# Optimization experiments

Measured on AMD Instinct MI355X. Metric: run time of the kernel, lower is better.

Reference implementation:

```python
import jax, jax.numpy as jnp
import numpy as np

N_NODES = 100000
N_EDGES = 640000
IN_FEATS = 128
OUT_FEATS = 128


def setup_inputs() -> dict:
    key = jax.random.key(0)
    k1, k2, k3 = jax.random.split(key, 3)
    feat = jax.random.normal(k1, (N_NODES, IN_FEATS), dtype=jnp.float32)
    edge_src = jax.random.randint(k2, (N_EDGES,), 0, N_NODES, dtype=jnp.int64)
    edge_dst = jax.random.randint(k3, (N_EDGES,), 0, N_NODES, dtype=jnp.int64)
    # init.constant_(weight, 1) / init.constant_(bias, 1) in the original module
    weight = jnp.ones((OUT_FEATS, IN_FEATS), dtype=jnp.float32)
    bias = jnp.ones((OUT_FEATS,), dtype=jnp.float32)
    return {"feat": feat, "edge_src": edge_src, "edge_dst": edge_dst,
            "weight": weight, "bias": bias}


def reference(feat, edge_src, edge_dst, weight, bias):
    # copy_u: message on each edge is the source node's feature  [E, F_in]
    msgs = feat[edge_src]
    # sum reduce messages into destination nodes                 [N_V, F_in]
    h = jax.ops.segment_sum(msgs, edge_dst, num_segments=N_NODES)
    # linear: h @ W^T + b                                        [N_V, F_out]
    return h @ weight.T + bias
```

## Files before the change

kernel.cpp:

```cpp
#include <hip/hip_runtime.h>

#define F 128
#define STRIDE 64

typedef __bf16 bf8 __attribute__((ext_vector_type(8)));
typedef __bf16 bf4 __attribute__((ext_vector_type(4)));
typedef float f4 __attribute__((ext_vector_type(4)));
typedef unsigned short us8 __attribute__((ext_vector_type(8)));

__global__ void zero_int(int* __restrict__ p, int n) {
  int i = blockIdx.x * blockDim.x + threadIdx.x;
  if (i < n) p[i] = 0;
}

__global__ void zero_f4(float4* __restrict__ p, int n4) {
  int i = blockIdx.x * blockDim.x + threadIdx.x;
  if (i < n4) p[i] = make_float4(0.f, 0.f, 0.f, 0.f);
}

__global__ __launch_bounds__(256, 2) void transform_and_build(
    const float* __restrict__ feat, const float* __restrict__ W,
    __bf16* __restrict__ tf, const int* __restrict__ esrc,
    const int* __restrict__ edst, int* __restrict__ cnt,
    int* __restrict__ bucket, int n_rows, int n_groups, int t_blocks,
    int b_blocks, int nE) {
  __shared__ bf8 wlds[2048];
  const int tid = threadIdx.x;

  if ((int)blockIdx.x >= t_blocks) {
    const int bbid = blockIdx.x - t_blocks;
    for (int e = bbid * 256 + tid; e < nE; e += b_blocks * 256) {
      int d = edst[e];
      int pos = atomicAdd(&cnt[d], 1);
      if (pos < STRIDE) bucket[(size_t)d * STRIDE + pos] = esrc[e];
    }
    return;
  }

  const int lane = tid & 63;
  const int wid = tid >> 6;
  const int lr = lane & 15;
  const int hi = lane >> 4;
  const int lk = hi * 8;

#pragma unroll
  for (int i = 0; i < 8; ++i) {
    int fid = tid + i * 256;
    int fl = fid & 63;
    int kkt = fid >> 6;
    int kk = kkt & 3;
    int t = kkt >> 2;
    const float* wr = W + (size_t)(t * 16 + (fl & 15)) * F + kk * 32 + (fl >> 4) * 8;
    float4 u0 = *(const float4*)wr;
    float4 u1 = *(const float4*)(wr + 4);
    bf8 b;
    b[0] = (__bf16)u0.x; b[1] = (__bf16)u0.y;
    b[2] = (__bf16)u0.z; b[3] = (__bf16)u0.w;
    b[4] = (__bf16)u1.x; b[5] = (__bf16)u1.y;
    b[6] = (__bf16)u1.z; b[7] = (__bf16)u1.w;
    wlds[fid] = b;
  }
  __syncthreads();

  for (int g = blockIdx.x; g < n_groups; g += t_blocks) {
    const int r0 = g * 64 + wid * 16;
    if (r0 >= n_rows) continue;
    int arow = r0 + lr;
    if (arow >= n_rows) arow = n_rows - 1;
    const float* hr = feat + (size_t)arow * F;
    bf8 af[4];
#pragma unroll
    for (int kk = 0; kk < 4; ++kk) {
      float4 u0 = *(const float4*)(hr + kk * 32 + lk);
      float4 u1 = *(const float4*)(hr + kk * 32 + lk + 4);
      bf8 a;
      a[0] = (__bf16)u0.x; a[1] = (__bf16)u0.y;
      a[2] = (__bf16)u0.z; a[3] = (__bf16)u0.w;
      a[4] = (__bf16)u1.x; a[5] = (__bf16)u1.y;
      a[6] = (__bf16)u1.z; a[7] = (__bf16)u1.w;
      af[kk] = a;
    }
    f4 acc[8];
#pragma unroll
    for (int t = 0; t < 8; ++t) acc[t] = (f4){0.f, 0.f, 0.f, 0.f};
#pragma unroll
    for (int kk = 0; kk < 4; ++kk)
#pragma unroll
      for (int t = 0; t < 8; ++t)
        acc[t] = __builtin_amdgcn_mfma_f32_16x16x32_bf16(
            wlds[(t * 4 + kk) * 64 + lane], af[kk], acc[t], 0, 0, 0);
    const int r = r0 + lr;
    if (r < n_rows) {
      __bf16* dst = tf + (size_t)r * F + hi * 4;
#pragma unroll
      for (int t = 0; t < 8; ++t) {
        bf4 p;
        p[0] = (__bf16)acc[t][0];
        p[1] = (__bf16)acc[t][1];
        p[2] = (__bf16)acc[t][2];
        p[3] = (__bf16)acc[t][3];
        *(bf4*)(dst + t * 16) = p;
      }
    }
  }
}

__global__ __launch_bounds__(256) void aggregate_bf16(
    const __bf16* __restrict__ tf, const int* __restrict__ cnt,
    const int* __restrict__ bucket, const float* __restrict__ bias,
    float* __restrict__ out, int n_nodes) {
  long long gid = (long long)blockIdx.x * 256 + threadIdx.x;
  int node = (int)(gid >> 4);
  int c = (int)(gid & 15);
  if (node >= n_nodes) return;
  int n = cnt[node];
  if (n > STRIDE) n = STRIDE;
  const int* eb = bucket + (size_t)node * STRIDE;
  const us8* t8 = (const us8*)tf;
  float4 b0 = ((const float4*)bias)[c * 2];
  float4 b1 = ((const float4*)bias)[c * 2 + 1];
  float a0 = b0.x, a1 = b0.y, a2 = b0.z, a3 = b0.w;
  float a4 = b1.x, a5 = b1.y, a6 = b1.z, a7 = b1.w;
  int k = 0;
  for (; k + 1 < n; k += 2) {
    int s0 = eb[k], s1 = eb[k + 1];
    us8 v0 = t8[(size_t)s0 * 16 + c];
    us8 v1 = t8[(size_t)s1 * 16 + c];
    a0 += __uint_as_float((unsigned)v0[0] << 16) + __uint_as_float((unsigned)v1[0] << 16);
    a1 += __uint_as_float((unsigned)v0[1] << 16) + __uint_as_float((unsigned)v1[1] << 16);
    a2 += __uint_as_float((unsigned)v0[2] << 16) + __uint_as_float((unsigned)v1[2] << 16);
    a3 += __uint_as_float((unsigned)v0[3] << 16) + __uint_as_float((unsigned)v1[3] << 16);
    a4 += __uint_as_float((unsigned)v0[4] << 16) + __uint_as_float((unsigned)v1[4] << 16);
    a5 += __uint_as_float((unsigned)v0[5] << 16) + __uint_as_float((unsigned)v1[5] << 16);
    a6 += __uint_as_float((unsigned)v0[6] << 16) + __uint_as_float((unsigned)v1[6] << 16);
    a7 += __uint_as_float((unsigned)v0[7] << 16) + __uint_as_float((unsigned)v1[7] << 16);
  }
  if (k < n) {
    us8 v0 = t8[(size_t)eb[k] * 16 + c];
    a0 += __uint_as_float((unsigned)v0[0] << 16);
    a1 += __uint_as_float((unsigned)v0[1] << 16);
    a2 += __uint_as_float((unsigned)v0[2] << 16);
    a3 += __uint_as_float((unsigned)v0[3] << 16);
    a4 += __uint_as_float((unsigned)v0[4] << 16);
    a5 += __uint_as_float((unsigned)v0[5] << 16);
    a6 += __uint_as_float((unsigned)v0[6] << 16);
    a7 += __uint_as_float((unsigned)v0[7] << 16);
  }
  float4* o = (float4*)out + (size_t)node * 32 + c * 2;
  o[0] = make_float4(a0, a1, a2, a3);
  o[1] = make_float4(a4, a5, a6, a7);
}

__global__ __launch_bounds__(256) void scatter_add(
    const float* __restrict__ feat, const int* __restrict__ src,
    const int* __restrict__ dst, float* __restrict__ h, int n_edges) {
  long long gid = (long long)blockIdx.x * 256 + threadIdx.x;
  int e = (int)(gid >> 5);
  if (e >= n_edges) return;
  int c = (int)(gid & 31);
  int s = src[e];
  int d = dst[e];
  float4 v = reinterpret_cast<const float4*>(feat + (long long)s * F)[c];
  float* hp = h + (long long)d * F + c * 4;
  __hip_atomic_fetch_add(hp + 0, v.x, __ATOMIC_RELAXED, __HIP_MEMORY_SCOPE_AGENT);
  __hip_atomic_fetch_add(hp + 1, v.y, __ATOMIC_RELAXED, __HIP_MEMORY_SCOPE_AGENT);
  __hip_atomic_fetch_add(hp + 2, v.z, __ATOMIC_RELAXED, __HIP_MEMORY_SCOPE_AGENT);
  __hip_atomic_fetch_add(hp + 3, v.w, __ATOMIC_RELAXED, __HIP_MEMORY_SCOPE_AGENT);
}

__global__ __launch_bounds__(256, 2) void gemm_bias_inplace(
    float* __restrict__ hout, const float* __restrict__ W,
    const float* __restrict__ bias, int n_rows, int n_groups) {
  const int lane = threadIdx.x & 63;
  const int wid = threadIdx.x >> 6;
  const int lr = lane & 15;
  const int lk = (lane >> 4) * 8;
  bf8 wf[8][4];
#pragma unroll
  for (int t = 0; t < 8; ++t) {
    const float* wr = W + (size_t)(t * 16 + lr) * F;
#pragma unroll
    for (int kk = 0; kk < 4; ++kk) {
      float4 u0 = *(const float4*)(wr + kk * 32 + lk);
      float4 u1 = *(const float4*)(wr + kk * 32 + lk + 4);
      bf8 b;
      b[0] = (__bf16)u0.x; b[1] = (__bf16)u0.y;
      b[2] = (__bf16)u0.z; b[3] = (__bf16)u0.w;
      b[4] = (__bf16)u1.x; b[5] = (__bf16)u1.y;
      b[6] = (__bf16)u1.z; b[7] = (__bf16)u1.w;
      wf[t][kk] = b;
    }
  }
  float bj[8];
#pragma unroll
  for (int t = 0; t < 8; ++t) bj[t] = bias[t * 16 + lr];
  for (int g = blockIdx.x; g < n_groups; g += gridDim.x) {
    const int r0 = g * 64 + wid * 16;
    if (r0 >= n_rows) continue;
    int arow = r0 + lr;
    if (arow >= n_rows) arow = n_rows - 1;
    const float* hr = hout + (size_t)arow * F;
    bf8 af[4];
#pragma unroll
    for (int kk = 0; kk < 4; ++kk) {
      float4 u0 = *(const float4*)(hr + kk * 32 + lk);
      float4 u1 = *(const float4*)(hr + kk * 32 + lk + 4);
      bf8 a;
      a[0] = (__bf16)u0.x; a[1] = (__bf16)u0.y;
      a[2] = (__bf16)u0.z; a[3] = (__bf16)u0.w;
      a[4] = (__bf16)u1.x; a[5] = (__bf16)u1.y;
      a[6] = (__bf16)u1.z; a[7] = (__bf16)u1.w;
      af[kk] = a;
    }
    f4 acc[8];
#pragma unroll
    for (int t = 0; t < 8; ++t) acc[t] = (f4){bj[t], bj[t], bj[t], bj[t]};
#pragma unroll
    for (int kk = 0; kk < 4; ++kk)
#pragma unroll
      for (int t = 0; t < 8; ++t)
        acc[t] = __builtin_amdgcn_mfma_f32_16x16x32_bf16(af[kk], wf[t][kk],
                                                         acc[t], 0, 0, 0);
    const int rbase = r0 + (lane >> 4) * 4;
#pragma unroll
    for (int t = 0; t < 8; ++t)
#pragma unroll
      for (int i = 0; i < 4; ++i) {
        int r = rbase + i;
        if (r < n_rows) hout[(size_t)r * F + t * 16 + lr] = acc[t][i];
      }
  }
}

static inline size_t align_up(size_t x, size_t a) { return (x + a - 1) & ~(a - 1); }

extern "C" void kernel_launch(void* const* d_in, const int* in_sizes, int n_in,
                              void* d_out, int out_size, void* d_ws, size_t ws_size,
                              hipStream_t stream) {
  const float* feat = (const float*)d_in[0];
  const int* esrc   = (const int*)d_in[1];
  const int* edst   = (const int*)d_in[2];
  const float* W    = (const float*)d_in[3];
  const float* bias = (const float*)d_in[4];
  float* out = (float*)d_out;

  const int nE = in_sizes[1];
  const int nN = out_size / F;

  size_t off_cnt  = 0;
  size_t off_bkt  = align_up(off_cnt + (size_t)nN * 4, 256);
  size_t off_tf   = align_up(off_bkt + (size_t)nN * STRIDE * 4, 256);
  size_t need     = off_tf + (size_t)nN * F * 2;
  const int n_groups = (nN + 63) / 64;

  if (ws_size >= need) {
    char* w = (char*)d_ws;
    int* cnt    = (int*)(w + off_cnt);
    int* bucket = (int*)(w + off_bkt);
    __bf16* tf  = (__bf16*)(w + off_tf);

    zero_int<<<(nN + 255) / 256, 256, 0, stream>>>(cnt, nN);

    const int t_blocks = (n_groups + 1) / 2;
    const int b_blocks = 128;
    transform_and_build<<<t_blocks + b_blocks, 256, 0, stream>>>(
        feat, W, tf, esrc, edst, cnt, bucket, nN, n_groups, t_blocks,
        b_blocks, nE);

    long long thr = (long long)nN * 16;
    aggregate_bf16<<<(int)((thr + 255) / 256), 256, 0, stream>>>(
        tf, cnt, bucket, bias, out, nN);
  } else {
    int n4 = out_size / 4;
    zero_f4<<<(n4 + 255) / 256, 256, 0, stream>>>((float4*)out, n4);
    long long total = (long long)nE * 32;
    scatter_add<<<(int)((total + 255) / 256), 256, 0, stream>>>(feat, esrc,
                                                                edst, out, nE);
    gemm_bias_inplace<<<640, 256, 0, stream>>>(out, W, bias, nN, n_groups);
  }
}
```

Before: 89.65 us.

## Split fused transform/bucket kernel into separate launches and prefetch feature rows

Replaces the single fused kernel, where some blocks built edge buckets while others ran a grid-strided bf16 MFMA transform, with two kernels. One is a one-thread-per-edge bucket build over a full grid, the other a one-group-per-block transform. The transform now issues the feature row loads before staging W into LDS, so global latency overlaps the weight conversion. This removes the load imbalance of only 128 bucket blocks running alongside the transform blocks, at the cost of an extra launch and no concurrency between the two phases.

```diff
diff --git a/kernel.cpp b/kernel.cpp
--- a/kernel.cpp
+++ b/kernel.cpp
@@ -18,30 +18,38 @@
   if (i < n4) p[i] = make_float4(0.f, 0.f, 0.f, 0.f);
 }
 
-__global__ __launch_bounds__(256, 2) void transform_and_build(
+__global__ __launch_bounds__(256) void build_bucket(
+    const int* __restrict__ esrc, const int* __restrict__ edst,
+    int* __restrict__ cnt, int* __restrict__ bucket, int nE) {
+  int e = blockIdx.x * 256 + threadIdx.x;
+  if (e >= nE) return;
+  int d = edst[e];
+  int pos = atomicAdd(&cnt[d], 1);
+  if (pos < STRIDE) bucket[(size_t)d * STRIDE + pos] = esrc[e];
+}
+
+__global__ __launch_bounds__(256, 2) void transform_bf16(
     const float* __restrict__ feat, const float* __restrict__ W,
-    __bf16* __restrict__ tf, const int* __restrict__ esrc,
-    const int* __restrict__ edst, int* __restrict__ cnt,
-    int* __restrict__ bucket, int n_rows, int n_groups, int t_blocks,
-    int b_blocks, int nE) {
+    __bf16* __restrict__ tf, int n_rows) {
   __shared__ bf8 wlds[2048];
   const int tid = threadIdx.x;
-
-  if ((int)blockIdx.x >= t_blocks) {
-    const int bbid = blockIdx.x - t_blocks;
-    for (int e = bbid * 256 + tid; e < nE; e += b_blocks * 256) {
-      int d = edst[e];
-      int pos = atomicAdd(&cnt[d], 1);
-      if (pos < STRIDE) bucket[(size_t)d * STRIDE + pos] = esrc[e];
-    }
-    return;
-  }
-
   const int lane = tid & 63;
   const int wid = tid >> 6;
   const int lr = lane & 15;
   const int hi = lane >> 4;
   const int lk = hi * 8;
+
+  const int r0 = blockIdx.x * 64 + wid * 16;
+  int arow = r0 + lr;
+  if (arow >= n_rows) arow = n_rows - 1;
+  const float* hr = feat + (size_t)arow * F;
+
+  float4 u[8];
+#pragma unroll
+  for (int kk = 0; kk < 4; ++kk) {
+    u[kk * 2]     = *(const float4*)(hr + kk * 32 + lk);
+    u[kk * 2 + 1] = *(const float4*)(hr + kk * 32 + lk + 4);
+  }
 
 #pragma unroll
   for (int i = 0; i < 8; ++i) {
@@ -51,56 +59,51 @@
     int kk = kkt & 3;
     int t = kkt >> 2;
     const float* wr = W + (size_t)(t * 16 + (fl & 15)) * F + kk * 32 + (fl >> 4) * 8;
-    float4 u0 = *(const float4*)wr;
-    float4 u1 = *(const float4*)(wr + 4);
+    float4 w0 = *(const float4*)wr;
+    float4 w1 = *(const float4*)(wr + 4);
     bf8 b;
-    b[0] = (__bf16)u0.x; b[1] = (__bf16)u0.y;
-    b[2] = (__bf16)u0.z; b[3] = (__bf16)u0.w;
-    b[4] = (__bf16)u1.x; b[5] = (__bf16)u1.y;
-    b[6] = (__bf16)u1.z; b[7] = (__bf16)u1.w;
+    b[0] = (__bf16)w0.x; b[1] = (__bf16)w0.y;
+    b[2] = (__bf16)w0.z; b[3] = (__bf16)w0.w;
+    b[4] = (__bf16)w1.x; b[5] = (__bf16)w1.y;
+    b[6] = (__bf16)w1.z; b[7] = (__bf16)w1.w;
     wlds[fid] = b;
   }
   __syncthreads();
 
-  for (int g = blockIdx.x; g < n_groups; g += t_blocks) {
-    const int r0 = g * 64 + wid * 16;
-    if (r0 >= n_rows) continue;
-    int arow = r0 + lr;
-    if (arow >= n_rows) arow = n_rows - 1;
-    const float* hr = feat + (size_t)arow * F;
-    bf8 af[4];
-#pragma unroll
-    for (int kk = 0; kk < 4; ++kk) {
-      float4 u0 = *(const float4*)(hr + kk * 32 + lk);
-      float4 u1 = *(const float4*)(hr + kk * 32 + lk + 4);
-      bf8 a;
-      a[0] = (__bf16)u0.x; a[1] = (__bf16)u0.y;
-      a[2] = (__bf16)u0.z; a[3] = (__bf16)u0.w;
-      a[4] = (__bf16)u1.x; a[5] = (__bf16)u1.y;
-      a[6] = (__bf16)u1.z; a[7] = (__bf16)u1.w;
-      af[kk] = a;
-    }
-    f4 acc[8];
-#pragma unroll
-    for (int t = 0; t < 8; ++t) acc[t] = (f4){0.f, 0.f, 0.f, 0.f};
-#pragma unroll
-    for (int kk = 0; kk < 4; ++kk)
-#pragma unroll
-      for (int t = 0; t < 8; ++t)
-        acc[t] = __builtin_amdgcn_mfma_f32_16x16x32_bf16(
-            wlds[(t * 4 + kk) * 64 + lane], af[kk], acc[t], 0, 0, 0);
-    const int r = r0 + lr;
-    if (r < n_rows) {
-      __bf16* dst = tf + (size_t)r * F + hi * 4;
-#pragma unroll
-      for (int t = 0; t < 8; ++t) {
-        bf4 p;
-        p[0] = (__bf16)acc[t][0];
-        p[1] = (__bf16)acc[t][1];
-        p[2] = (__bf16)acc[t][2];
-        p[3] = (__bf16)acc[t][3];
-        *(bf4*)(dst + t * 16) = p;
-      }
+  if (r0 >= n_rows) return;
+
+  bf8 af[4];
+#pragma unroll
+  for (int kk = 0; kk < 4; ++kk) {
+    bf8 a;
+    a[0] = (__bf16)u[kk * 2].x;     a[1] = (__bf16)u[kk * 2].y;
+    a[2] = (__bf16)u[kk * 2].z;     a[3] = (__bf16)u[kk * 2].w;
+    a[4] = (__bf16)u[kk * 2 + 1].x; a[5] = (__bf16)u[kk * 2 + 1].y;
+    a[6] = (__bf16)u[kk * 2 + 1].z; a[7] = (__bf16)u[kk * 2 + 1].w;
+    af[kk] = a;
+  }
+
+  f4 acc[8];
+#pragma unroll
+  for (int t = 0; t < 8; ++t) acc[t] = (f4){0.f, 0.f, 0.f, 0.f};
+#pragma unroll
+  for (int kk = 0; kk < 4; ++kk)
+#pragma unroll
+    for (int t = 0; t < 8; ++t)
+      acc[t] = __builtin_amdgcn_mfma_f32_16x16x32_bf16(
+          wlds[(t * 4 + kk) * 64 + lane], af[kk], acc[t], 0, 0, 0);
+
+  const int r = r0 + lr;
+  if (r < n_rows) {
+    __bf16* dst = tf + (size_t)r * F + hi * 4;
+#pragma unroll
+    for (int t = 0; t < 8; ++t) {
+      bf4 p;
+      p[0] = (__bf16)acc[t][0];
+      p[1] = (__bf16)acc[t][1];
+      p[2] = (__bf16)acc[t][2];
+      p[3] = (__bf16)acc[t][3];
+      *(bf4*)(dst + t * 16) = p;
     }
   }
 }
@@ -260,12 +263,9 @@
     __bf16* tf  = (__bf16*)(w + off_tf);
 
     zero_int<<<(nN + 255) / 256, 256, 0, stream>>>(cnt, nN);
-
-    const int t_blocks = (n_groups + 1) / 2;
-    const int b_blocks = 128;
-    transform_and_build<<<t_blocks + b_blocks, 256, 0, stream>>>(
-        feat, W, tf, esrc, edst, cnt, bucket, nN, n_groups, t_blocks,
-        b_blocks, nE);
+    build_bucket<<<(nE + 255) / 256, 256, 0, stream>>>(esrc, edst, cnt,
+                                                       bucket, nE);
+    transform_bf16<<<n_groups, 256, 0, stream>>>(feat, W, tf, nN);
 
     long long thr = (long long)nN * 16;
     aggregate_bf16<<<(int)((thr + 255) / 256), 256, 0, stream>>>(
```

Result: slower. 102.0 us (+13.8%).
